# Kernel optimization log

Hardware: AMD Instinct MI355X
Metric: run time of the kernel (lower is better)

Reference implementation:

```python
import jax, jax.numpy as jnp
import numpy as np

NUM_ATOMS = 4_000_000
NUM_TYPES = 11

def setup_inputs() -> dict:
    key = jax.random.key(0)
    k1, k2 = jax.random.split(key)
    input_coords = jax.random.normal(k1, (3 * NUM_ATOMS,), dtype=jnp.float32)
    atom_types = jax.random.randint(k2, (NUM_ATOMS,), 0, NUM_TYPES, dtype=jnp.int64)
    return {"input_coords": input_coords, "atom_types": atom_types, "num_atom_types": NUM_TYPES}

def reference(input_coords, atom_types, num_atom_types):
    # counts per atom type  [T]
    counts = jnp.bincount(atom_types, length=num_atom_types).astype(jnp.int32)
    # exclusive prefix sum -> bucket offsets  [T]
    offsets = (jnp.cumsum(counts) - counts).astype(jnp.int32)
    # stable sort by type reproduces the C++ bucket fill order:
    # atoms of the same type keep their original relative order.
    perm = jnp.argsort(atom_types, stable=True)  # [N] source index for each output slot
    coords3 = input_coords.reshape(-1, 3)        # [N,3]
    typed_coords = coords3[perm].reshape(-1)     # [3N] type-grouped flat coords
    return typed_coords, counts, offsets
```

## Files before the change

### kernel.cpp

```cpp
#include <hip/hip_runtime.h>

#define NTYPES 11
#define BLOCK  256
#define ITEMS  8
#define CHUNK  (BLOCK * ITEMS)
#define MAXCH  32

__global__ __launch_bounds__(BLOCK) void hist_kernel(
    const int* __restrict__ types, int N, int B, int* __restrict__ bc) {
  __shared__ int shCnt[NTYPES];
  const int tid = threadIdx.x;
  const int b = blockIdx.x;
  if (tid < NTYPES) shCnt[tid] = 0;
  __syncthreads();

  const int run = b * CHUNK + tid * ITEMS;
  int cnt[NTYPES];
#pragma unroll
  for (int t = 0; t < NTYPES; ++t) cnt[t] = 0;

  if (run < N) {
    const int4* p = (const int4*)(types + run);
    int4 a0 = p[0], a1 = p[1];
    int ty[ITEMS] = {a0.x, a0.y, a0.z, a0.w, a1.x, a1.y, a1.z, a1.w};
#pragma unroll
    for (int k = 0; k < ITEMS; ++k) {
#pragma unroll
      for (int t = 0; t < NTYPES; ++t) cnt[t] += (ty[k] == t) ? 1 : 0;
    }
  }

  const int lane = tid & 63;
#pragma unroll
  for (int t = 0; t < NTYPES; ++t) {
    int v = cnt[t];
    for (int o = 32; o >= 1; o >>= 1) v += __shfl_down(v, o);
    if (lane == 0) atomicAdd(&shCnt[t], v);
  }
  __syncthreads();
  if (tid < NTYPES) bc[tid * B + b] = shCnt[tid];
}

__global__ __launch_bounds__(NTYPES * 64) void scan_kernel(
    const int* __restrict__ bc, int B, int* __restrict__ scanOut,
    int* __restrict__ offs, float* __restrict__ outTail) {
  __shared__ int totals[NTYPES];
  const int lane = threadIdx.x & 63;
  const int t = threadIdx.x >> 6;
  const int nch = (B + 63) >> 6;

  int x[MAXCH];
#pragma unroll
  for (int c = 0; c < MAXCH; ++c) {
    const int idx = c * 64 + lane;
    x[c] = (c < nch && idx < B) ? bc[t * B + idx] : 0;
  }

  int carry = 0;
#pragma unroll
  for (int c = 0; c < MAXCH; ++c) {
    if (c >= nch) break;
    int incl = x[c];
#pragma unroll
    for (int o = 1; o < 64; o <<= 1) {
      int v = __shfl_up(incl, o);
      if (lane >= o) incl += v;
    }
    incl += carry;
    const int idx = c * 64 + lane;
    if (idx < B) scanOut[t * B + idx] = incl - x[c];
    carry = __shfl(incl, 63);
  }
  if (lane == 0) totals[t] = carry;
  __syncthreads();

  if (threadIdx.x == 0) {
    int off = 0;
    for (int u = 0; u < NTYPES; ++u) {
      const int c = totals[u];
      offs[u] = off;
      outTail[u] = (float)c;
      outTail[NTYPES + u] = (float)off;
      off += c;
    }
  }
}

__global__ __launch_bounds__(BLOCK) void scatter_kernel(
    const float* __restrict__ coords, const int* __restrict__ types,
    const int* __restrict__ scanOut, const int* __restrict__ offs, int N,
    int B, float* __restrict__ out) {
  __shared__ float shC[CHUNK * 3];
  __shared__ int wtot[NTYPES][4];
  __shared__ int shOff[NTYPES + 1];
  __shared__ int shDelta[NTYPES];

  const int tid = threadIdx.x;
  const int b = blockIdx.x;
  const int lane = tid & 63;
  const int wave = tid >> 6;
  const int run = b * CHUNK + tid * ITEMS;
  const bool active = (run < N);

  int ty[ITEMS];
  int cnt[NTYPES];
#pragma unroll
  for (int t = 0; t < NTYPES; ++t) cnt[t] = 0;
#pragma unroll
  for (int k = 0; k < ITEMS; ++k) ty[k] = -1;

  float c[ITEMS * 3];
  if (active) {
    const int4* p = (const int4*)(types + run);
    int4 a0 = p[0], a1 = p[1];
    int tt[ITEMS] = {a0.x, a0.y, a0.z, a0.w, a1.x, a1.y, a1.z, a1.w};
#pragma unroll
    for (int k = 0; k < ITEMS; ++k) ty[k] = tt[k];
    const float4* cp = (const float4*)(coords + (size_t)run * 3);
#pragma unroll
    for (int q = 0; q < (ITEMS * 3) / 4; ++q) {
      float4 v = cp[q];
      c[4 * q + 0] = v.x;
      c[4 * q + 1] = v.y;
      c[4 * q + 2] = v.z;
      c[4 * q + 3] = v.w;
    }
#pragma unroll
    for (int k = 0; k < ITEMS; ++k) {
#pragma unroll
      for (int t = 0; t < NTYPES; ++t) cnt[t] += (ty[k] == t) ? 1 : 0;
    }
  }

  int rank[NTYPES];
#pragma unroll
  for (int t = 0; t < NTYPES; ++t) {
    int incl = cnt[t];
#pragma unroll
    for (int o = 1; o < 64; o <<= 1) {
      int v = __shfl_up(incl, o);
      if (lane >= o) incl += v;
    }
    if (lane == 63) wtot[t][wave] = incl;
    rank[t] = incl - cnt[t];
  }
  __syncthreads();

  if (tid < NTYPES) {
    int loc = 0;
    for (int u = 0; u < tid; ++u)
      loc += wtot[u][0] + wtot[u][1] + wtot[u][2] + wtot[u][3];
    shOff[tid] = loc;
    shDelta[tid] = 3 * (offs[tid] + scanOut[tid * B + b] - loc);
    if (tid == NTYPES - 1) {
      shOff[NTYPES] =
          loc + wtot[tid][0] + wtot[tid][1] + wtot[tid][2] + wtot[tid][3];
    }
  }
  __syncthreads();

#pragma unroll
  for (int t = 0; t < NTYPES; ++t) {
    int wb = 0;
#pragma unroll
    for (int w = 0; w < 3; ++w) wb += (w < wave) ? wtot[t][w] : 0;
    rank[t] += wb + shOff[t];
  }

  if (active) {
#pragma unroll
    for (int k = 0; k < ITEMS; ++k) {
      const int t0 = ty[k];
      int slot = 0;
#pragma unroll
      for (int t = 0; t < NTYPES; ++t) {
        if (t0 == t) {
          slot = rank[t];
          rank[t] += 1;
        }
      }
      shC[3 * slot + 0] = c[3 * k + 0];
      shC[3 * slot + 1] = c[3 * k + 1];
      shC[3 * slot + 2] = c[3 * k + 2];
    }
  }
  __syncthreads();

  const int total = shOff[NTYPES];
  int offr[NTYPES];
  int dlt[NTYPES];
#pragma unroll
  for (int t = 0; t < NTYPES; ++t) {
    offr[t] = shOff[t];
    dlt[t] = shDelta[t];
  }
#pragma unroll
  for (int k = 0; k < ITEMS; ++k) {
    const int s = k * BLOCK + tid;
    if (s < total) {
      int d = dlt[0];
#pragma unroll
      for (int t = 1; t < NTYPES; ++t) d = (s >= offr[t]) ? dlt[t] : d;
      const int src = 3 * s;
      out[src + d + 0] = shC[src + 0];
      out[src + d + 1] = shC[src + 1];
      out[src + d + 2] = shC[src + 2];
    }
  }
}

extern "C" void kernel_launch(void* const* d_in, const int* in_sizes, int n_in,
                              void* d_out, int out_size, void* d_ws,
                              size_t ws_size, hipStream_t stream) {
  const float* coords = (const float*)d_in[0];
  const int* types = (const int*)d_in[1];
  const int N = in_sizes[1];
  const int B = (N + CHUNK - 1) / CHUNK;

  int* bc = (int*)d_ws;
  int* scanOut = bc + NTYPES * B;
  int* offs = scanOut + NTYPES * B;
  float* out = (float*)d_out;
  float* outTail = out + (size_t)3 * N;

  hist_kernel<<<B, BLOCK, 0, stream>>>(types, N, B, bc);
  scan_kernel<<<1, NTYPES * 64, 0, stream>>>(bc, B, scanOut, offs, outTail);
  scatter_kernel<<<B, BLOCK, 0, stream>>>(coords, types, scanOut, offs, N, B,
                                          out);
}
```

Before: 135.7 us.

## Pack atom types to 4 bits in histogram pass and gather coords via LDS permutation

The histogram kernel now writes each thread's eight types packed into one 32-bit word. The scatter kernel reads that packed word instead of reloading the full int type array, cutting type-read traffic in the second pass. Instead of staging coordinates in LDS, the scatter builds a 16-bit local permutation in LDS and then gathers coordinates directly from global memory per output slot. This cuts LDS use, which may raise occupancy, but turns the coalesced float4 coordinate loads into scattered, uncoalesced 4-byte reads. It also adds a small write of the packed array in the histogram kernel.

```diff
diff --git a/kernel.cpp b/kernel.cpp
--- a/kernel.cpp
+++ b/kernel.cpp
@@ -7,7 +7,8 @@
 #define MAXCH  32
 
 __global__ __launch_bounds__(BLOCK) void hist_kernel(
-    const int* __restrict__ types, int N, int B, int* __restrict__ bc) {
+    const int* __restrict__ types, int N, int B, int* __restrict__ bc,
+    unsigned int* __restrict__ packed) {
   __shared__ int shCnt[NTYPES];
   const int tid = threadIdx.x;
   const int b = blockIdx.x;
@@ -23,6 +24,10 @@
     const int4* p = (const int4*)(types + run);
     int4 a0 = p[0], a1 = p[1];
     int ty[ITEMS] = {a0.x, a0.y, a0.z, a0.w, a1.x, a1.y, a1.z, a1.w};
+    unsigned int pk = 0;
+#pragma unroll
+    for (int k = 0; k < ITEMS; ++k) pk |= ((unsigned int)ty[k]) << (4 * k);
+    packed[b * BLOCK + tid] = pk;
 #pragma unroll
     for (int k = 0; k < ITEMS; ++k) {
 #pragma unroll
@@ -87,10 +92,10 @@
 }
 
 __global__ __launch_bounds__(BLOCK) void scatter_kernel(
-    const float* __restrict__ coords, const int* __restrict__ types,
+    const float* __restrict__ coords, const unsigned int* __restrict__ packed,
     const int* __restrict__ scanOut, const int* __restrict__ offs, int N,
     int B, float* __restrict__ out) {
-  __shared__ float shC[CHUNK * 3];
+  __shared__ unsigned short perm[CHUNK];
   __shared__ int wtot[NTYPES][4];
   __shared__ int shOff[NTYPES + 1];
   __shared__ int shDelta[NTYPES];
@@ -109,22 +114,10 @@
 #pragma unroll
   for (int k = 0; k < ITEMS; ++k) ty[k] = -1;
 
-  float c[ITEMS * 3];
   if (active) {
-    const int4* p = (const int4*)(types + run);
-    int4 a0 = p[0], a1 = p[1];
-    int tt[ITEMS] = {a0.x, a0.y, a0.z, a0.w, a1.x, a1.y, a1.z, a1.w};
-#pragma unroll
-    for (int k = 0; k < ITEMS; ++k) ty[k] = tt[k];
-    const float4* cp = (const float4*)(coords + (size_t)run * 3);
-#pragma unroll
-    for (int q = 0; q < (ITEMS * 3) / 4; ++q) {
-      float4 v = cp[q];
-      c[4 * q + 0] = v.x;
-      c[4 * q + 1] = v.y;
-      c[4 * q + 2] = v.z;
-      c[4 * q + 3] = v.w;
-    }
+    const unsigned int pk = packed[b * BLOCK + tid];
+#pragma unroll
+    for (int k = 0; k < ITEMS; ++k) ty[k] = (int)((pk >> (4 * k)) & 0xFu);
 #pragma unroll
     for (int k = 0; k < ITEMS; ++k) {
 #pragma unroll
@@ -179,9 +172,7 @@
           rank[t] += 1;
         }
       }
-      shC[3 * slot + 0] = c[3 * k + 0];
-      shC[3 * slot + 1] = c[3 * k + 1];
-      shC[3 * slot + 2] = c[3 * k + 2];
+      perm[slot] = (unsigned short)(tid * ITEMS + k);
     }
   }
   __syncthreads();
@@ -194,17 +185,20 @@
     offr[t] = shOff[t];
     dlt[t] = shDelta[t];
   }
+  const float* cbase = coords + (size_t)b * CHUNK * 3;
 #pragma unroll
   for (int k = 0; k < ITEMS; ++k) {
     const int s = k * BLOCK + tid;
     if (s < total) {
+      const int li = (int)perm[s];
       int d = dlt[0];
 #pragma unroll
       for (int t = 1; t < NTYPES; ++t) d = (s >= offr[t]) ? dlt[t] : d;
-      const int src = 3 * s;
-      out[src + d + 0] = shC[src + 0];
-      out[src + d + 1] = shC[src + 1];
-      out[src + d + 2] = shC[src + 2];
+      const int src = 3 * li;
+      const int dst = 3 * s + d;
+      out[dst + 0] = cbase[src + 0];
+      out[dst + 1] = cbase[src + 1];
+      out[dst + 2] = cbase[src + 2];
     }
   }
 }
@@ -220,11 +214,12 @@
   int* bc = (int*)d_ws;
   int* scanOut = bc + NTYPES * B;
   int* offs = scanOut + NTYPES * B;
+  unsigned int* packed = (unsigned int*)(offs + NTYPES + 1);
   float* out = (float*)d_out;
   float* outTail = out + (size_t)3 * N;
 
-  hist_kernel<<<B, BLOCK, 0, stream>>>(types, N, B, bc);
+  hist_kernel<<<B, BLOCK, 0, stream>>>(types, N, B, bc, packed);
   scan_kernel<<<1, NTYPES * 64, 0, stream>>>(bc, B, scanOut, offs, outTail);
-  scatter_kernel<<<B, BLOCK, 0, stream>>>(coords, types, scanOut, offs, N, B,
+  scatter_kernel<<<B, BLOCK, 0, stream>>>(coords, packed, scanOut, offs, N, B,
                                           out);
 }
```

New measurement: 150.8 us. 1.11x slower.
